# Optimization experiments

Measured on AMD Instinct MI355X. Metric: run time of the kernel, lower is better.

## Reference

```python
import jax, jax.numpy as jnp
import numpy as np


def setup_inputs() -> dict:
    key = jax.random.key(0)
    ks = jax.random.split(key, 9)
    B, N, E = 4, 100000, 400000
    Dv = De = Dc = 64
    Din, H, Dout = De + 2 * Dv + Dc, 128, 64  # 256, 128, 64
    return {
        "vdata": jax.random.normal(ks[0], (B, N, Dv), dtype=jnp.float32),
        "edata": jax.random.normal(ks[1], (B, E, De), dtype=jnp.float32),
        "cdata": jax.random.normal(ks[2], (B, Dc), dtype=jnp.float32),
        "W1": jax.random.normal(ks[3], (Din, H), dtype=jnp.float32) * (1.0 / np.sqrt(Din)),
        "b1": jnp.zeros((H,), dtype=jnp.float32),
        "W2": jax.random.normal(ks[4], (H, Dout), dtype=jnp.float32) * (1.0 / np.sqrt(H)),
        "b2": jnp.zeros((Dout,), dtype=jnp.float32),
        "sender_ids": jax.random.randint(ks[5], (B, E), 0, N, dtype=jnp.int64 if jax.config.jax_enable_x64 else jnp.int32).astype(jnp.int32),
        "receiver_ids": jax.random.randint(ks[6], (B, E), 0, N, dtype=jnp.int64 if jax.config.jax_enable_x64 else jnp.int32).astype(jnp.int32),
    }


def reference(vdata, edata, cdata, W1, b1, W2, b2, sender_ids, receiver_ids):
    # Gather sender/receiver vertex features per edge: [B,E,Dv]
    gather = jax.vmap(lambda v, idx: v[idx])  # per-graph gather along node dim
    sender_data = gather(vdata, sender_ids)
    receiver_data = gather(vdata, receiver_ids)
    B, E = edata.shape[0], edata.shape[1]
    # Context repeated per edge: [B,E,Dc]
    ctx = jnp.broadcast_to(cdata[:, None, :], (B, E, cdata.shape[-1]))
    # etin = cat(edge, sender, receiver, context) along feature dim -> [B,E,256]
    etin = jnp.concatenate([edata, sender_data, receiver_data, ctx], axis=2)
    # Batched MLP updater
    h = jax.nn.relu(jnp.einsum("bei,ih->beh", etin, W1) + b1)
    out = jnp.einsum("beh,ho->beo", h, W2) + b2
    return out
```

## Files before the change

### kernel.cpp

```cpp
#include <hip/hip_runtime.h>

typedef __attribute__((ext_vector_type(8))) __bf16 bf16x8;
typedef __attribute__((ext_vector_type(4))) float f32x4;
typedef __attribute__((ext_vector_type(4))) unsigned int u32x4;

#define NV 100000
#define NE 400000
#define NT (NE / 32)

#define W1T_OFF 0
#define W2T_OFF 65536
#define LDS_SIZE 81920

__device__ inline unsigned short f2b_rne(float f) {
    unsigned u = __builtin_bit_cast(unsigned, f);
    return (unsigned short)((u + 0x7fffu + ((u >> 16) & 1u)) >> 16);
}

__device__ inline unsigned pk2(float lo, float hi) {
    unsigned r;
    asm("v_cvt_pk_bf16_f32 %0, %1, %2" : "=v"(r) : "v"(lo), "v"(hi));
    return r;
}

__device__ inline bf16x8 pack8(f32x4 a, f32x4 b) {
    u32x4 u = {pk2(a[0], a[1]), pk2(a[2], a[3]), pk2(b[0], b[1]), pk2(b[2], b[3])};
    return __builtin_bit_cast(bf16x8, u);
}

__device__ inline f32x4 ldv(const float* p) { return *(const f32x4*)p; }

__device__ inline bf16x8 load8(const float* p) {
    f32x4 x = *(const f32x4*)p;
    f32x4 y = *(const f32x4*)(p + 4);
    return pack8(x, y);
}

__global__ __launch_bounds__(512, 4) void edgeblock_kernel(
    const float* __restrict__ vdata, const float* __restrict__ edata,
    const float* __restrict__ cdata, const float* __restrict__ W1,
    const float* __restrict__ b1, const float* __restrict__ W2,
    const float* __restrict__ b2, const int* __restrict__ snd,
    const int* __restrict__ rcv, float* __restrict__ out)
{
    __shared__ __align__(16) unsigned char lds[LDS_SIZE];
    const int tid = threadIdx.x;
    const int lane = tid & 63;
    const int w = tid >> 6;
    const int l15 = lane & 15;
    const int lg = lane >> 4;

    const int bid = blockIdx.x;
    const int xcd = bid & 7;
    const int b   = xcd >> 1;
    const int blk = ((bid >> 3) << 1) | (xcd & 1);

    for (int i = tid; i < 256 * 128; i += 512) {
        int k = i >> 7, n = i & 127;
        *(unsigned short*)(lds + W1T_OFF + n * 512 + ((k * 2) ^ ((n & 7) << 4))) = f2b_rne(W1[i]);
    }
    for (int i = tid; i < 128 * 64; i += 512) {
        int k = i >> 6, n = i & 63;
        int kc2 = k >> 5, c = k & 31;
        int j   = ((c >> 4) << 2) | (c & 3);
        int lgs = (c >> 2) & 3;
        int off = kc2 * 64 + lgs * 16 + j * 2;
        *(unsigned short*)(lds + W2T_OFF + n * 256 + (off ^ ((n & 7) << 4))) = f2b_rne(W2[i]);
    }
    __syncthreads();

    const float* cd = cdata + b * 64;
    const bf16x8 cfr0 = load8(cd + lg * 8);
    const bf16x8 cfr1 = load8(cd + 32 + lg * 8);

    const size_t bE = (size_t)b * NE;
    const float* ed_b = edata + bE * 64;
    const float* vd_b = vdata + (size_t)b * NV * 64;
    const int* snd_b = snd + bE;
    const int* rcv_b = rcv + bE;
    float* out_b = out + bE * 64;

    for (int t = blk * 8 + w; t < NT; t += 1024) {
        const int e0 = t * 32;
        const int sid0 = snd_b[e0 + l15], sid1 = snd_b[e0 + 16 + l15];
        const int rid0 = rcv_b[e0 + l15], rid1 = rcv_b[e0 + 16 + l15];

        const float* er0 = ed_b + (size_t)(e0 + l15) * 64 + lg * 8;
        const float* er1 = er0 + 16 * 64;
        const float* sr0 = vd_b + (size_t)sid0 * 64 + lg * 8;
        const float* sr1 = vd_b + (size_t)sid1 * 64 + lg * 8;
        const float* rr0 = vd_b + (size_t)rid0 * 64 + lg * 8;
        const float* rr1 = vd_b + (size_t)rid1 * 64 + lg * 8;

        bf16x8 af[6][2];
        af[0][0] = load8(er0);      af[0][1] = load8(er1);
        af[1][0] = load8(er0 + 32); af[1][1] = load8(er1 + 32);
        af[2][0] = load8(sr0);      af[2][1] = load8(sr1);
        af[3][0] = load8(sr0 + 32); af[3][1] = load8(sr1 + 32);
        af[4][0] = load8(rr0);      af[4][1] = load8(rr1);
        af[5][0] = load8(rr0 + 32); af[5][1] = load8(rr1 + 32);

        f32x4 acc1[8][2];
#pragma unroll
        for (int ht = 0; ht < 8; ++ht) {
            f32x4 bv = ldv(b1 + ht * 16 + lg * 4);
            acc1[ht][0] = bv; acc1[ht][1] = bv;
        }

#pragma unroll
        for (int kc = 0; kc < 8; ++kc) {
            bf16x8 bc0, bc1;
            if (kc < 6)      { bc0 = af[kc][0]; bc1 = af[kc][1]; }
            else if (kc == 6){ bc0 = cfr0;      bc1 = cfr0; }
            else             { bc0 = cfr1;      bc1 = cfr1; }
#pragma unroll
            for (int ht = 0; ht < 8; ++ht) {
                const int row = ht * 16 + l15;
                const bf16x8 wf = *(const bf16x8*)(lds + W1T_OFF + row * 512 +
                                                   ((kc * 64 + lg * 16) ^ ((row & 7) << 4)));
                acc1[ht][0] = __builtin_amdgcn_mfma_f32_16x16x32_bf16(wf, bc0, acc1[ht][0], 0, 0, 0);
                acc1[ht][1] = __builtin_amdgcn_mfma_f32_16x16x32_bf16(wf, bc1, acc1[ht][1], 0, 0, 0);
            }
        }

        bf16x8 q[2][4];
#pragma unroll
        for (int kc2 = 0; kc2 < 4; ++kc2)
#pragma unroll
            for (int et = 0; et < 2; ++et) {
                f32x4 u = acc1[2 * kc2][et], v = acc1[2 * kc2 + 1][et];
                u32x4 pq;
                pq[0] = pk2(fmaxf(u[0], 0.f), fmaxf(u[1], 0.f));
                pq[1] = pk2(fmaxf(u[2], 0.f), fmaxf(u[3], 0.f));
                pq[2] = pk2(fmaxf(v[0], 0.f), fmaxf(v[1], 0.f));
                pq[3] = pk2(fmaxf(v[2], 0.f), fmaxf(v[3], 0.f));
                q[et][kc2] = __builtin_bit_cast(bf16x8, pq);
            }

        f32x4 acc2[4][2];
#pragma unroll
        for (int dt = 0; dt < 4; ++dt) {
            f32x4 bv = ldv(b2 + dt * 16 + lg * 4);
            acc2[dt][0] = bv; acc2[dt][1] = bv;
        }
#pragma unroll
        for (int kc2 = 0; kc2 < 4; ++kc2)
#pragma unroll
            for (int dt = 0; dt < 4; ++dt) {
                const int row = dt * 16 + l15;
                const bf16x8 wf = *(const bf16x8*)(lds + W2T_OFF + row * 256 +
                                                   ((kc2 * 64 + lg * 16) ^ ((row & 7) << 4)));
                acc2[dt][0] = __builtin_amdgcn_mfma_f32_16x16x32_bf16(wf, q[0][kc2], acc2[dt][0], 0, 0, 0);
                acc2[dt][1] = __builtin_amdgcn_mfma_f32_16x16x32_bf16(wf, q[1][kc2], acc2[dt][1], 0, 0, 0);
            }

        float* ob0 = out_b + (size_t)(e0 + l15) * 64 + lg * 4;
        float* ob1 = ob0 + 16 * 64;
#pragma unroll
        for (int dt = 0; dt < 4; ++dt) {
            *(f32x4*)(ob0 + dt * 16) = acc2[dt][0];
            *(f32x4*)(ob1 + dt * 16) = acc2[dt][1];
        }
    }
}

extern "C" void kernel_launch(void* const* d_in, const int* in_sizes, int n_in,
                              void* d_out, int out_size, void* d_ws, size_t ws_size,
                              hipStream_t stream) {
    const float* vdata = (const float*)d_in[0];
    const float* edata = (const float*)d_in[1];
    const float* cdata = (const float*)d_in[2];
    const float* W1    = (const float*)d_in[3];
    const float* b1    = (const float*)d_in[4];
    const float* W2    = (const float*)d_in[5];
    const float* b2    = (const float*)d_in[6];
    const int*   snd   = (const int*)d_in[7];
    const int*   rcv   = (const int*)d_in[8];
    float* out = (float*)d_out;

    edgeblock_kernel<<<dim3(512), dim3(512), 0, stream>>>(
        vdata, edata, cdata, W1, b1, W2, b2, snd, rcv, out);
}
```

Baseline: 336.0 us.

## Pre-convert vertex table to bf16 and use nontemporal edge loads

Adds a pre-pass kernel that converts the whole vertex feature table to bf16 in the workspace, so the random sender/receiver gathers in the main kernel fetch half the bytes per row. Edge feature loads are switched to nontemporal loads so the streamed edge data is less likely to evict the gathered vertex rows from cache. The cost is an extra full pass over vdata (read 102MB, write 51MB) on every call. A fallback path keeps the fp32 gather when the workspace is too small.

```diff
diff --git a/kernel.cpp b/kernel.cpp
--- a/kernel.cpp
+++ b/kernel.cpp
@@ -7,6 +7,9 @@
 #define NV 100000
 #define NE 400000
 #define NT (NE / 32)
+
+#define VTAB_ELEMS ((size_t)4 * NV * 64)
+#define VTAB_BYTES (VTAB_ELEMS * 2)
 
 #define W1T_OFF 0
 #define W2T_OFF 65536
@@ -29,6 +32,7 @@
 }
 
 __device__ inline f32x4 ldv(const float* p) { return *(const f32x4*)p; }
+__device__ inline f32x4 ntl(const float* p) { return __builtin_nontemporal_load((const f32x4*)p); }
 
 __device__ inline bf16x8 load8(const float* p) {
     f32x4 x = *(const f32x4*)p;
@@ -36,8 +40,22 @@
     return pack8(x, y);
 }
 
+__global__ __launch_bounds__(256) void vconv_kernel(const float* __restrict__ vdata,
+                                                    unsigned short* __restrict__ vt)
+{
+    const size_t G = VTAB_ELEMS / 8;
+    for (size_t g = (size_t)blockIdx.x * blockDim.x + threadIdx.x; g < G;
+         g += (size_t)gridDim.x * blockDim.x) {
+        const float* p = vdata + g * 8;
+        f32x4 a = ldv(p), b = ldv(p + 4);
+        *(bf16x8*)(vt + g * 8) = pack8(a, b);
+    }
+}
+
+template <int BF16V>
 __global__ __launch_bounds__(512, 4) void edgeblock_kernel(
-    const float* __restrict__ vdata, const float* __restrict__ edata,
+    const float* __restrict__ vdata, const unsigned short* __restrict__ vt,
+    const float* __restrict__ edata,
     const float* __restrict__ cdata, const float* __restrict__ W1,
     const float* __restrict__ b1, const float* __restrict__ W2,
     const float* __restrict__ b2, const int* __restrict__ snd,
@@ -76,6 +94,7 @@
     const size_t bE = (size_t)b * NE;
     const float* ed_b = edata + bE * 64;
     const float* vd_b = vdata + (size_t)b * NV * 64;
+    const unsigned short* vt_b = vt + (size_t)b * NV * 64;
     const int* snd_b = snd + bE;
     const int* rcv_b = rcv + bE;
     float* out_b = out + bE * 64;
@@ -87,18 +106,31 @@
 
         const float* er0 = ed_b + (size_t)(e0 + l15) * 64 + lg * 8;
         const float* er1 = er0 + 16 * 64;
-        const float* sr0 = vd_b + (size_t)sid0 * 64 + lg * 8;
-        const float* sr1 = vd_b + (size_t)sid1 * 64 + lg * 8;
-        const float* rr0 = vd_b + (size_t)rid0 * 64 + lg * 8;
-        const float* rr1 = vd_b + (size_t)rid1 * 64 + lg * 8;
 
         bf16x8 af[6][2];
-        af[0][0] = load8(er0);      af[0][1] = load8(er1);
-        af[1][0] = load8(er0 + 32); af[1][1] = load8(er1 + 32);
-        af[2][0] = load8(sr0);      af[2][1] = load8(sr1);
-        af[3][0] = load8(sr0 + 32); af[3][1] = load8(sr1 + 32);
-        af[4][0] = load8(rr0);      af[4][1] = load8(rr1);
-        af[5][0] = load8(rr0 + 32); af[5][1] = load8(rr1 + 32);
+        af[0][0] = pack8(ntl(er0), ntl(er0 + 4));
+        af[0][1] = pack8(ntl(er1), ntl(er1 + 4));
+        af[1][0] = pack8(ntl(er0 + 32), ntl(er0 + 36));
+        af[1][1] = pack8(ntl(er1 + 32), ntl(er1 + 36));
+        if constexpr (BF16V) {
+            const unsigned short* s0 = vt_b + (size_t)sid0 * 64 + lg * 8;
+            const unsigned short* s1 = vt_b + (size_t)sid1 * 64 + lg * 8;
+            const unsigned short* r0 = vt_b + (size_t)rid0 * 64 + lg * 8;
+            const unsigned short* r1 = vt_b + (size_t)rid1 * 64 + lg * 8;
+            af[2][0] = *(const bf16x8*)(s0);      af[2][1] = *(const bf16x8*)(s1);
+            af[3][0] = *(const bf16x8*)(s0 + 32); af[3][1] = *(const bf16x8*)(s1 + 32);
+            af[4][0] = *(const bf16x8*)(r0);      af[4][1] = *(const bf16x8*)(r1);
+            af[5][0] = *(const bf16x8*)(r0 + 32); af[5][1] = *(const bf16x8*)(r1 + 32);
+        } else {
+            const float* sr0 = vd_b + (size_t)sid0 * 64 + lg * 8;
+            const float* sr1 = vd_b + (size_t)sid1 * 64 + lg * 8;
+            const float* rr0 = vd_b + (size_t)rid0 * 64 + lg * 8;
+            const float* rr1 = vd_b + (size_t)rid1 * 64 + lg * 8;
+            af[2][0] = load8(sr0);      af[2][1] = load8(sr1);
+            af[3][0] = load8(sr0 + 32); af[3][1] = load8(sr1 + 32);
+            af[4][0] = load8(rr0);      af[4][1] = load8(rr1);
+            af[5][0] = load8(rr0 + 32); af[5][1] = load8(rr1 + 32);
+        }
 
         f32x4 acc1[8][2];
 #pragma unroll
@@ -178,6 +210,13 @@
     const int*   rcv   = (const int*)d_in[8];
     float* out = (float*)d_out;
 
-    edgeblock_kernel<<<dim3(512), dim3(512), 0, stream>>>(
-        vdata, edata, cdata, W1, b1, W2, b2, snd, rcv, out);
-}
+    if (ws_size >= VTAB_BYTES) {
+        unsigned short* vt = (unsigned short*)d_ws;
+        vconv_kernel<<<dim3(2048), dim3(256), 0, stream>>>(vdata, vt);
+        edgeblock_kernel<1><<<dim3(512), dim3(512), 0, stream>>>(
+            vdata, vt, edata, cdata, W1, b1, W2, b2, snd, rcv, out);
+    } else {
+        edgeblock_kernel<0><<<dim3(512), dim3(512), 0, stream>>>(
+            vdata, (const unsigned short*)d_ws, edata, cdata, W1, b1, W2, b2, snd, rcv, out);
+    }
+}
```

New measurement: 311.4 us. -7.3%, faster.

## Pre-convert vertex table to bf16, fold context into bias, pipeline edge loads

Applied to the files above, without the earlier changes.

Adds a pre-pass that converts vertex features to a bf16 table in workspace and a tiny kernel that folds the constant context contribution into a per-graph hidden bias, shrinking the first GEMM K dimension from 256 to 192. The main kernel now software-pipelines the next tile's edge, index and gather loads behind current MFMA work and uses nontemporal loads for streamed edge data. This aims to halve gather bytes and hide memory latency, at the cost of an extra full pass over vertex data per call and dependence on workspace size (falls back to the old kernel otherwise).

```diff
diff --git a/kernel.cpp b/kernel.cpp
--- a/kernel.cpp
+++ b/kernel.cpp
@@ -7,6 +7,10 @@
 #define NV 100000
 #define NE 400000
 #define NT (NE / 32)
+
+#define VTAB_ELEMS ((size_t)4 * NV * 64)
+#define VTAB_BYTES (VTAB_ELEMS * 2)
+#define WS_NEED (VTAB_BYTES + 2048)
 
 #define W1T_OFF 0
 #define W2T_OFF 65536
@@ -29,6 +33,7 @@
 }
 
 __device__ inline f32x4 ldv(const float* p) { return *(const f32x4*)p; }
+__device__ inline f32x4 ntl(const float* p) { return __builtin_nontemporal_load((const f32x4*)p); }
 
 __device__ inline bf16x8 load8(const float* p) {
     f32x4 x = *(const f32x4*)p;
@@ -36,7 +41,189 @@
     return pack8(x, y);
 }
 
+__global__ __launch_bounds__(256) void vconv_kernel(const float* __restrict__ vdata,
+                                                    unsigned short* __restrict__ vt)
+{
+    const size_t G = VTAB_ELEMS / 8;
+    for (size_t g = (size_t)blockIdx.x * blockDim.x + threadIdx.x; g < G;
+         g += (size_t)gridDim.x * blockDim.x) {
+        const float* p = vdata + g * 8;
+        *(bf16x8*)(vt + g * 8) = pack8(ldv(p), ldv(p + 4));
+    }
+}
+
+__global__ __launch_bounds__(512) void hc_kernel(const float* __restrict__ W1,
+                                                 const float* __restrict__ b1,
+                                                 const float* __restrict__ cdata,
+                                                 float* __restrict__ hc)
+{
+    const int tid = threadIdx.x;
+    const int b = tid >> 7, hid = tid & 127;
+    float s = b1[hid];
+#pragma unroll 8
+    for (int j = 0; j < 64; ++j)
+        s += cdata[b * 64 + j] * W1[(192 + j) * 128 + hid];
+    hc[b * 128 + hid] = s;
+}
+
+
+#define L1STEP(KC, BC0, BC1) \
+  { _Pragma("unroll") \
+    for (int ht = 0; ht < 8; ++ht) { \
+      const int row = ht * 16 + l15; \
+      const bf16x8 wf = *(const bf16x8*)(lds + W1T_OFF + row * 512 + \
+          (((KC) * 64 + lg * 16) ^ ((row & 7) << 4))); \
+      acc1[ht][0] = __builtin_amdgcn_mfma_f32_16x16x32_bf16(wf, BC0, acc1[ht][0], 0, 0, 0); \
+      acc1[ht][1] = __builtin_amdgcn_mfma_f32_16x16x32_bf16(wf, BC1, acc1[ht][1], 0, 0, 0); \
+    } }
+
+#define ED_ISSUE(T) { \
+    const float* ep0_ = ed_b + (size_t)((T) * 32 + l15) * 64 + lg * 8; \
+    const float* ep1_ = ep0_ + 16 * 64; \
+    f0 = ntl(ep0_); f1 = ntl(ep0_ + 4); f4 = ntl(ep0_ + 32); f5 = ntl(ep0_ + 36); \
+    f2 = ntl(ep1_); f3 = ntl(ep1_ + 4); f6 = ntl(ep1_ + 32); f7 = ntl(ep1_ + 36); }
+
+#define VT_ISSUE() { \
+    const unsigned short* s0_ = vt_b + (size_t)sN0 * 64 + lg * 8; \
+    const unsigned short* s1_ = vt_b + (size_t)sN1 * 64 + lg * 8; \
+    const unsigned short* r0_ = vt_b + (size_t)rN0 * 64 + lg * 8; \
+    const unsigned short* r1_ = vt_b + (size_t)rN1 * 64 + lg * 8; \
+    a20 = *(const bf16x8*)(s0_);      a21 = *(const bf16x8*)(s1_); \
+    a30 = *(const bf16x8*)(s0_ + 32); a31 = *(const bf16x8*)(s1_ + 32); \
+    a40 = *(const bf16x8*)(r0_);      a41 = *(const bf16x8*)(r1_); \
+    a50 = *(const bf16x8*)(r0_ + 32); a51 = *(const bf16x8*)(r1_ + 32); }
+
+#define IDX_LOAD(T) { \
+    const int e_ = (T) * 32; \
+    sN0 = snd_b[e_ + l15]; sN1 = snd_b[e_ + 16 + l15]; \
+    rN0 = rcv_b[e_ + l15]; rN1 = rcv_b[e_ + 16 + l15]; }
+
 __global__ __launch_bounds__(512, 4) void edgeblock_kernel(
+    const unsigned short* __restrict__ vt, const float* __restrict__ hc,
+    const float* __restrict__ edata, const float* __restrict__ W1,
+    const float* __restrict__ W2, const float* __restrict__ b2,
+    const int* __restrict__ snd, const int* __restrict__ rcv,
+    float* __restrict__ out)
+{
+    __shared__ __align__(16) unsigned char lds[LDS_SIZE];
+    const int tid = threadIdx.x;
+    const int lane = tid & 63;
+    const int w = tid >> 6;
+    const int l15 = lane & 15;
+    const int lg = lane >> 4;
+
+    const int bid = blockIdx.x;
+    const int xcd = bid & 7;
+    const int b   = xcd >> 1;
+    const int blk = ((bid >> 3) << 1) | (xcd & 1);
+
+    for (int i = tid; i < 192 * 128; i += 512) {
+        int k = i >> 7, n = i & 127;
+        *(unsigned short*)(lds + W1T_OFF + n * 512 + ((k * 2) ^ ((n & 7) << 4))) = f2b_rne(W1[i]);
+    }
+    for (int i = tid; i < 128 * 64; i += 512) {
+        int k = i >> 6, n = i & 63;
+        int kc2 = k >> 5, c = k & 31;
+        int j   = ((c >> 4) << 2) | (c & 3);
+        int lgs = (c >> 2) & 3;
+        int off = kc2 * 64 + lgs * 16 + j * 2;
+        *(unsigned short*)(lds + W2T_OFF + n * 256 + (off ^ ((n & 7) << 4))) = f2b_rne(W2[i]);
+    }
+    __syncthreads();
+
+    const size_t bE = (size_t)b * NE;
+    const float* ed_b = edata + bE * 64;
+    const unsigned short* vt_b = vt + (size_t)b * NV * 64;
+    const float* hc_b = hc + b * 128;
+    const int* snd_b = snd + bE;
+    const int* rcv_b = rcv + bE;
+    float* out_b = out + bE * 64;
+
+    int t = blk * 8 + w;
+    bf16x8 a20, a21, a30, a31, a40, a41, a50, a51;
+    f32x4 f0, f1, f2, f3, f4, f5, f6, f7;
+    int sN0, sN1, rN0, rN1;
+
+    IDX_LOAD(t);
+    ED_ISSUE(t);
+    VT_ISSUE();
+    int tn = t + 1024;
+    bool more = tn < NT;
+    IDX_LOAD(more ? tn : t);
+
+    for (;;) {
+        bf16x8 a00 = pack8(f0, f1), a01 = pack8(f2, f3);
+        bf16x8 a10 = pack8(f4, f5), a11 = pack8(f6, f7);
+
+        f32x4 acc1[8][2];
+#pragma unroll
+        for (int ht = 0; ht < 8; ++ht) {
+            f32x4 bv = ldv(hc_b + ht * 16 + lg * 4);
+            acc1[ht][0] = bv; acc1[ht][1] = bv;
+        }
+
+        if (more) ED_ISSUE(tn);
+
+        L1STEP(0, a00, a01)
+        L1STEP(1, a10, a11)
+        L1STEP(2, a20, a21)
+        L1STEP(3, a30, a31)
+        L1STEP(4, a40, a41)
+        L1STEP(5, a50, a51)
+
+        if (more) {
+            VT_ISSUE();
+            const int tq = tn + 1024;
+            IDX_LOAD(tq < NT ? tq : tn);
+        }
+
+        bf16x8 q[2][4];
+#pragma unroll
+        for (int kc2 = 0; kc2 < 4; ++kc2)
+#pragma unroll
+            for (int et = 0; et < 2; ++et) {
+                f32x4 u = acc1[2 * kc2][et], v = acc1[2 * kc2 + 1][et];
+                u32x4 pq;
+                pq[0] = pk2(fmaxf(u[0], 0.f), fmaxf(u[1], 0.f));
+                pq[1] = pk2(fmaxf(u[2], 0.f), fmaxf(u[3], 0.f));
+                pq[2] = pk2(fmaxf(v[0], 0.f), fmaxf(v[1], 0.f));
+                pq[3] = pk2(fmaxf(v[2], 0.f), fmaxf(v[3], 0.f));
+                q[et][kc2] = __builtin_bit_cast(bf16x8, pq);
+            }
+
+        f32x4 acc2[4][2];
+#pragma unroll
+        for (int dt = 0; dt < 4; ++dt) {
+            f32x4 bv = ldv(b2 + dt * 16 + lg * 4);
+            acc2[dt][0] = bv; acc2[dt][1] = bv;
+        }
+#pragma unroll
+        for (int kc2 = 0; kc2 < 4; ++kc2)
+#pragma unroll
+            for (int dt = 0; dt < 4; ++dt) {
+                const int row = dt * 16 + l15;
+                const bf16x8 wf = *(const bf16x8*)(lds + W2T_OFF + row * 256 +
+                                                   ((kc2 * 64 + lg * 16) ^ ((row & 7) << 4)));
+                acc2[dt][0] = __builtin_amdgcn_mfma_f32_16x16x32_bf16(wf, q[0][kc2], acc2[dt][0], 0, 0, 0);
+                acc2[dt][1] = __builtin_amdgcn_mfma_f32_16x16x32_bf16(wf, q[1][kc2], acc2[dt][1], 0, 0, 0);
+            }
+
+        {
+            float* ob0 = out_b + (size_t)(t * 32 + l15) * 64 + lg * 4;
+            float* ob1 = ob0 + 16 * 64;
+#pragma unroll
+            for (int dt = 0; dt < 4; ++dt) {
+                *(f32x4*)(ob0 + dt * 16) = acc2[dt][0];
+                *(f32x4*)(ob1 + dt * 16) = acc2[dt][1];
+            }
+        }
+
+        if (!more) break;
+        t = tn; tn += 1024; more = tn < NT;
+    }
+}
+
+__global__ __launch_bounds__(512, 4) void edgeblock_legacy(
     const float* __restrict__ vdata, const float* __restrict__ edata,
     const float* __restrict__ cdata, const float* __restrict__ W1,
     const float* __restrict__ b1, const float* __restrict__ W2,
@@ -49,7 +236,6 @@
     const int w = tid >> 6;
     const int l15 = lane & 15;
     const int lg = lane >> 4;
-
     const int bid = blockIdx.x;
     const int xcd = bid & 7;
     const int b   = xcd >> 1;
@@ -84,7 +270,6 @@
         const int e0 = t * 32;
         const int sid0 = snd_b[e0 + l15], sid1 = snd_b[e0 + 16 + l15];
         const int rid0 = rcv_b[e0 + l15], rid1 = rcv_b[e0 + 16 + l15];
-
         const float* er0 = ed_b + (size_t)(e0 + l15) * 64 + lg * 8;
         const float* er1 = er0 + 16 * 64;
         const float* sr0 = vd_b + (size_t)sid0 * 64 + lg * 8;
@@ -106,7 +291,6 @@
             f32x4 bv = ldv(b1 + ht * 16 + lg * 4);
             acc1[ht][0] = bv; acc1[ht][1] = bv;
         }
-
 #pragma unroll
         for (int kc = 0; kc < 8; ++kc) {
             bf16x8 bc0, bc1;
@@ -178,6 +362,15 @@
     const int*   rcv   = (const int*)d_in[8];
     float* out = (float*)d_out;
 
-    edgeblock_kernel<<<dim3(512), dim3(512), 0, stream>>>(
-        vdata, edata, cdata, W1, b1, W2, b2, snd, rcv, out);
-}
+    if (ws_size >= WS_NEED) {
+        unsigned short* vt = (unsigned short*)d_ws;
+        float* hc = (float*)((char*)d_ws + VTAB_BYTES);
+        vconv_kernel<<<dim3(2048), dim3(256), 0, stream>>>(vdata, vt);
+        hc_kernel<<<dim3(1), dim3(512), 0, stream>>>(W1, b1, cdata, hc);
+        edgeblock_kernel<<<dim3(512), dim3(512), 0, stream>>>(
+            vt, hc, edata, W1, W2, b2, snd, rcv, out);
+    } else {
+        edgeblock_legacy<<<dim3(512), dim3(512), 0, stream>>>(
+            vdata, edata, cdata, W1, b1, W2, b2, snd, rcv, out);
+    }
+}
```

Result: slower. 547.2 us (+62.9%).
